# Performance work log

Hardware: AMD Instinct MI355X
Metric: run time of the kernel (lower is better)

## Reference

```python
import jax, jax.numpy as jnp
import numpy as np


def euler_xyz_to_matrix(angles):
    # pytorch3d euler_angles_to_matrix(angles, 'XYZ') = R_X(a0) @ R_Y(a1) @ R_Z(a2)
    ax, ay, az = angles[..., 0], angles[..., 1], angles[..., 2]
    cx, sx = jnp.cos(ax), jnp.sin(ax)
    cy, sy = jnp.cos(ay), jnp.sin(ay)
    cz, sz = jnp.cos(az), jnp.sin(az)
    one = jnp.ones_like(ax)
    zero = jnp.zeros_like(ax)
    Rx = jnp.stack([one, zero, zero, zero, cx, -sx, zero, sx, cx], axis=-1).reshape(*ax.shape, 3, 3)
    Ry = jnp.stack([cy, zero, sy, zero, one, zero, -sy, zero, cy], axis=-1).reshape(*ax.shape, 3, 3)
    Rz = jnp.stack([cz, -sz, zero, sz, cz, zero, zero, zero, one], axis=-1).reshape(*ax.shape, 3, 3)
    return Rx @ Ry @ Rz


def chamfer_bidir(x, y):
    # x, y: [R, I, N, 3]. Squared-distance chamfer, mean point reduction, per (R,I) batch.
    x2 = jnp.sum(x * x, axis=-1)  # [R,I,N]
    y2 = jnp.sum(y * y, axis=-1)  # [R,I,N]
    # d2[r,i,n,m] = |x_n - y_m|^2
    d2 = x2[..., :, None] + y2[..., None, :] - 2.0 * jnp.einsum('rind,rimd->rinm', x, y)
    cham_x = jnp.mean(jnp.min(d2, axis=-1), axis=-1)  # x -> nearest y
    cham_y = jnp.mean(jnp.min(d2, axis=-2), axis=-1)  # y -> nearest x
    return cham_x + cham_y  # [R, I]


def setup_inputs() -> dict:
    key = jax.random.key(0)
    k1, k2, k3, k4 = jax.random.split(key, 4)
    R, I, N = 4, 16, 2048
    source_points = jax.random.normal(k1, (R, I, N, 3), dtype=jnp.float32)
    target_points = jax.random.normal(k2, (I, N, 3), dtype=jnp.float32)
    rotation = 0.1 * jax.random.normal(k3, (R, I, 3), dtype=jnp.float32)
    translation = 0.1 * jax.random.normal(k4, (R, I, 3), dtype=jnp.float32)
    scale = jnp.ones((R, I), dtype=jnp.float32)
    return {
        'source_points': source_points,
        'target_points': target_points,
        'rotation': rotation,
        'translation': translation,
        'scale': scale,
    }


def reference(source_points, target_points, rotation, translation, scale):
    R, I, N, _ = source_points.shape
    rot = euler_xyz_to_matrix(rotation)  # [R,I,3,3]
    # Transform per original: 4x4 matrix with rows [:3,:] scaled by `scale`,
    # so p' = scale * (rot @ p + translation).
    transformed = scale[..., None, None] * (
        jnp.einsum('rind,rikd->rink', source_points, rot) + translation[..., None, :]
    )  # [R,I,N,3]
    # target_points [I,N,3] broadcast to [R,I,N,3] (original repeats along R)
    target = jnp.broadcast_to(target_points[None], transformed.shape)
    # original calls chamfer_distance(target, transformed): x=target, y=transformed
    return chamfer_bidir(target, transformed)  # [R, I]
```

## Files before the change

kernel.cpp:

```cpp
#include <hip/hip_runtime.h>
#include <math.h>

#define RDIM 4
#define IDIM 16
#define NPAIR 64
#define NPTS 2048
#define THREADS 256
#define ROWSB 256
#define RBLK (NPTS / ROWSB)
#define TILES (NPTS / 32)
#define SCRS 68
#define ONEBF 0x3F80u

typedef __attribute__((ext_vector_type(8))) short bf16x8;
typedef __attribute__((ext_vector_type(16))) float f32x16;
typedef __attribute__((ext_vector_type(4))) float f32x4;

__device__ __forceinline__ unsigned int f2bf(float f) {
    union { float f; unsigned int u; } v; v.f = f;
    return (v.u + 0x7FFFu + ((v.u >> 16) & 1u)) >> 16;
}
__device__ __forceinline__ float bf2f(unsigned int h) {
    union { unsigned int u; float f; } v; v.u = h << 16; return v.f;
}

__device__ __forceinline__ void make_rot(const float* __restrict__ rotv, int pair,
                                         float& r00, float& r01, float& r02,
                                         float& r10, float& r11, float& r12,
                                         float& r20, float& r21, float& r22) {
    const float ax = rotv[pair * 3 + 0];
    const float ay = rotv[pair * 3 + 1];
    const float az = rotv[pair * 3 + 2];
    float sx, cx, sy, cy, sz, cz;
    sincosf(ax, &sx, &cx);
    sincosf(ay, &sy, &cy);
    sincosf(az, &sz, &cz);
    r00 = cy * cz;                r01 = -cy * sz;               r02 = sy;
    r10 = cx * sz + sx * sy * cz; r11 = cx * cz - sx * sy * sz; r12 = -sx * cy;
    r20 = sx * sz - cx * sy * cz; r21 = sx * cz + cx * sy * sz; r22 = cx * cy;
}

__device__ __forceinline__ uint4 brec(float v0, float v1, float v2) {
    const float b0 = -2.0f * v0, b1 = -2.0f * v1, b2 = -2.0f * v2;
    const unsigned int h0 = f2bf(b0), h1 = f2bf(b1), h2 = f2bf(b2);
    const unsigned int l0 = f2bf(b0 - bf2f(h0));
    const unsigned int l1 = f2bf(b1 - bf2f(h1));
    const unsigned int l2 = f2bf(b2 - bf2f(h2));
    const float n2 = v0 * v0 + v1 * v1 + v2 * v2;
    const unsigned int nh = f2bf(n2), nl = f2bf(n2 - bf2f(nh));
    return make_uint4(h0 | (h1 << 16), h2 | (l0 << 16), l1 | (l2 << 16), nh | (nl << 16));
}
__device__ __forceinline__ void arec(float q0, float q1, float q2, uint4& a0, uint4& a1) {
    const unsigned int h0 = f2bf(q0), h1 = f2bf(q1), h2 = f2bf(q2);
    const unsigned int l0 = f2bf(q0 - bf2f(h0));
    const unsigned int l1 = f2bf(q1 - bf2f(h1));
    const unsigned int l2 = f2bf(q2 - bf2f(h2));
    a0 = make_uint4(h0 | (h1 << 16), h2 | (l0 << 16), l1 | (l2 << 16), ONEBF);
    a1 = make_uint4(l0 | (l1 << 16), l2 | (h0 << 16), h1 | (h2 << 16), ONEBF << 16);
}

__global__ __launch_bounds__(THREADS)
void prep(const float* __restrict__ src, const float* __restrict__ tgt,
          const float* __restrict__ rotv, const float* __restrict__ trav,
          const float* __restrict__ scal,
          uint4* __restrict__ Yb, uint4* __restrict__ Ya,
          uint4* __restrict__ Xb, uint4* __restrict__ Xa)
{
    const int b = blockIdx.x;
    const int tid = threadIdx.x;
    if (b < NPAIR) {
        const int pair = b;
        float r00, r01, r02, r10, r11, r12, r20, r21, r22;
        make_rot(rotv, pair, r00, r01, r02, r10, r11, r12, r20, r21, r22);
        const float t0 = trav[pair * 3 + 0];
        const float t1 = trav[pair * 3 + 1];
        const float t2 = trav[pair * 3 + 2];
        const float s  = scal[pair];
        const float* __restrict__ srcp = src + (size_t)pair * NPTS * 3;
#pragma unroll
        for (int u = 0; u < NPTS / THREADS; ++u) {
            const int m = u * THREADS + tid;
            const float p0 = srcp[m * 3 + 0];
            const float p1 = srcp[m * 3 + 1];
            const float p2 = srcp[m * 3 + 2];
            const float y0 = s * fmaf(r00, p0, fmaf(r01, p1, fmaf(r02, p2, t0)));
            const float y1 = s * fmaf(r10, p0, fmaf(r11, p1, fmaf(r12, p2, t1)));
            const float y2 = s * fmaf(r20, p0, fmaf(r21, p1, fmaf(r22, p2, t2)));
            Yb[(size_t)pair * NPTS + m] = brec(y0, y1, y2);
            uint4 a0, a1;
            arec(y0, y1, y2, a0, a1);
            Ya[((size_t)pair * NPTS + m) * 2 + 0] = a0;
            Ya[((size_t)pair * NPTS + m) * 2 + 1] = a1;
        }
    } else {
        const int i = b - NPAIR;
        const float* __restrict__ tgtp = tgt + (size_t)i * NPTS * 3;
#pragma unroll
        for (int u = 0; u < NPTS / THREADS; ++u) {
            const int m = u * THREADS + tid;
            const float x0 = tgtp[m * 3 + 0];
            const float x1 = tgtp[m * 3 + 1];
            const float x2 = tgtp[m * 3 + 2];
            Xb[(size_t)i * NPTS + m] = brec(x0, x1, x2);
            uint4 a0, a1;
            arec(x0, x1, x2, a0, a1);
            Xa[((size_t)i * NPTS + m) * 2 + 0] = a0;
            Xa[((size_t)i * NPTS + m) * 2 + 1] = a1;
        }
    }
}

__global__ __launch_bounds__(THREADS, 3)
void chamfer_main(const uint4* __restrict__ Yb, const uint4* __restrict__ Ya,
                  const uint4* __restrict__ Xb, const uint4* __restrict__ Xa,
                  float* __restrict__ out)
{
    __shared__ alignas(16) unsigned char smem[34816 + 8192];
    __shared__ float wsum[4];
    unsigned short* sB = (unsigned short*)smem;
    float* scratch = (float*)smem;
    unsigned short* sA = (unsigned short*)(smem + 34816);

    const int pair  = blockIdx.x;
    const int rb    = blockIdx.y;
    const int passB = blockIdx.z;
    const int i     = pair & (IDIM - 1);
    const int tid   = threadIdx.x;
    const int lane  = tid & 63;
    const int w     = tid >> 6;
    const int c31   = lane & 31;
    const int h     = lane >> 5;

    const uint4* __restrict__ gB = (passB == 0) ? (Yb + (size_t)pair * NPTS)
                                                : (Xb + (size_t)i * NPTS);
    const uint4* __restrict__ gA = (passB == 0)
        ? (Xa + ((size_t)i * NPTS + rb * ROWSB) * 2)
        : (Ya + ((size_t)pair * NPTS + rb * ROWSB) * 2);

#pragma unroll
    for (int j = 0; j < 8; ++j)
        ((uint4*)sB)[j * THREADS + tid] = gB[j * THREADS + tid];
    ((uint4*)sA)[tid] = gA[tid];
    ((uint4*)sA)[THREADS + tid] = gA[THREADS + tid];
    __syncthreads();

    bf16x8 af[2];
    af[0] = *(const bf16x8*)&sA[(w * 64 + c31) * 16 + h * 8];
    af[1] = *(const bf16x8*)&sA[(w * 64 + 32 + c31) * 16 + h * 8];

    float mn[2][16];
#pragma unroll
    for (int rt = 0; rt < 2; ++rt)
#pragma unroll
        for (int j = 0; j < 16; ++j) mn[rt][j] = 3.4e38f;

    const f32x16 zero16 = {0,0,0,0, 0,0,0,0, 0,0,0,0, 0,0,0,0};

#pragma unroll 4
    for (int t = 0; t < TILES; ++t) {
        const bf16x8 bf = *(const bf16x8*)&sB[(t * 32 + c31) * 8];
        const f32x16 d0 = __builtin_amdgcn_mfma_f32_32x32x16_bf16(af[0], bf, zero16, 0, 0, 0);
        const f32x16 d1 = __builtin_amdgcn_mfma_f32_32x32x16_bf16(af[1], bf, zero16, 0, 0, 0);
#pragma unroll
        for (int j = 0; j < 16; ++j) {
            mn[0][j] = fminf(mn[0][j], d0[j]);
            mn[1][j] = fminf(mn[1][j], d1[j]);
        }
    }
    __syncthreads();

#pragma unroll
    for (int rt = 0; rt < 2; ++rt)
#pragma unroll
        for (int g2 = 0; g2 < 4; ++g2) {
            const int rowb = rt * 32 + 8 * g2 + 4 * h;
            f32x4 v4;
            v4[0] = mn[rt][g2 * 4 + 0];
            v4[1] = mn[rt][g2 * 4 + 1];
            v4[2] = mn[rt][g2 * 4 + 2];
            v4[3] = mn[rt][g2 * 4 + 3];
            *(f32x4*)&scratch[(w * 32 + c31) * SCRS + rowb] = v4;
        }
    __syncthreads();

    float m = scratch[(w * 32) * SCRS + lane];
#pragma unroll
    for (int c = 1; c < 32; ++c)
        m = fminf(m, scratch[(w * 32 + c) * SCRS + lane]);

    const unsigned short* ar = &sA[tid * 16];
    const float q0 = bf2f(ar[0]) + bf2f(ar[3]);
    const float q1 = bf2f(ar[1]) + bf2f(ar[4]);
    const float q2 = bf2f(ar[2]) + bf2f(ar[5]);
    float v = m + q0 * q0 + q1 * q1 + q2 * q2;

#pragma unroll
    for (int off = 32; off > 0; off >>= 1)
        v += __shfl_down(v, off, 64);
    if (lane == 0) wsum[w] = v;
    __syncthreads();
    if (tid == 0) {
        const float tot = wsum[0] + wsum[1] + wsum[2] + wsum[3];
        atomicAdd(&out[pair], tot * (1.0f / NPTS));
    }
}

extern "C" void kernel_launch(void* const* d_in, const int* in_sizes, int n_in,
                              void* d_out, int out_size, void* d_ws, size_t ws_size,
                              hipStream_t stream) {
    const float* src  = (const float*)d_in[0];
    const float* tgt  = (const float*)d_in[1];
    const float* rotv = (const float*)d_in[2];
    const float* trav = (const float*)d_in[3];
    const float* scal = (const float*)d_in[4];
    float* out = (float*)d_out;

    char* ws = (char*)d_ws;
    uint4* Yb = (uint4*)ws;
    uint4* Ya = (uint4*)(ws + (size_t)NPAIR * NPTS * 16);
    uint4* Xb = (uint4*)(ws + (size_t)NPAIR * NPTS * 48);
    uint4* Xa = (uint4*)(ws + (size_t)NPAIR * NPTS * 48 + (size_t)IDIM * NPTS * 16);

    hipMemsetAsync(out, 0, NPAIR * sizeof(float), stream);

    prep<<<NPAIR + IDIM, THREADS, 0, stream>>>(src, tgt, rotv, trav, scal, Yb, Ya, Xb, Xa);

    dim3 grid(NPAIR, RBLK, 2);
    chamfer_main<<<grid, THREADS, 0, stream>>>(Yb, Ya, Xb, Xa, out);
}
```

Baseline: 86.91 us.

## Split prep across more blocks, raise occupancy, pair MFMA tiles with min3, swizzle scratch

The prep kernel is split into four segments per batch so more blocks participate in the transform and bf16 packing. The main kernel shrinks the scratch stride to 64 and uses an XOR swizzle to avoid LDS bank conflicts, which lets shared memory drop enough to target four blocks per CU. The inner loop processes two tiles per iteration and folds them with three-input min to cut VALU min ops. Requesting higher occupancy may push register pressure and risk spills.

```diff
diff --git a/kernel.cpp b/kernel.cpp
--- a/kernel.cpp
+++ b/kernel.cpp
@@ -9,12 +9,17 @@
 #define ROWSB 256
 #define RBLK (NPTS / ROWSB)
 #define TILES (NPTS / 32)
-#define SCRS 68
+#define SCRS 64
+#define PSPLIT 4
 #define ONEBF 0x3F80u
 
 typedef __attribute__((ext_vector_type(8))) short bf16x8;
 typedef __attribute__((ext_vector_type(16))) float f32x16;
 typedef __attribute__((ext_vector_type(4))) float f32x4;
+
+__device__ __forceinline__ float min3f(float a, float b, float c) {
+    return fminf(a, fminf(b, c));
+}
 
 __device__ __forceinline__ unsigned int f2bf(float f) {
     union { float f; unsigned int u; } v; v.f = f;
@@ -66,8 +71,10 @@
           uint4* __restrict__ Yb, uint4* __restrict__ Ya,
           uint4* __restrict__ Xb, uint4* __restrict__ Xa)
 {
-    const int b = blockIdx.x;
+    const int b   = blockIdx.x;
+    const int seg = blockIdx.y;
     const int tid = threadIdx.x;
+    const int m0  = seg * (NPTS / PSPLIT);
     if (b < NPAIR) {
         const int pair = b;
         float r00, r01, r02, r10, r11, r12, r20, r21, r22;
@@ -78,8 +85,8 @@
         const float s  = scal[pair];
         const float* __restrict__ srcp = src + (size_t)pair * NPTS * 3;
 #pragma unroll
-        for (int u = 0; u < NPTS / THREADS; ++u) {
-            const int m = u * THREADS + tid;
+        for (int u = 0; u < NPTS / THREADS / PSPLIT; ++u) {
+            const int m = m0 + u * THREADS + tid;
             const float p0 = srcp[m * 3 + 0];
             const float p1 = srcp[m * 3 + 1];
             const float p2 = srcp[m * 3 + 2];
@@ -96,8 +103,8 @@
         const int i = b - NPAIR;
         const float* __restrict__ tgtp = tgt + (size_t)i * NPTS * 3;
 #pragma unroll
-        for (int u = 0; u < NPTS / THREADS; ++u) {
-            const int m = u * THREADS + tid;
+        for (int u = 0; u < NPTS / THREADS / PSPLIT; ++u) {
+            const int m = m0 + u * THREADS + tid;
             const float x0 = tgtp[m * 3 + 0];
             const float x1 = tgtp[m * 3 + 1];
             const float x2 = tgtp[m * 3 + 2];
@@ -110,16 +117,16 @@
     }
 }
 
-__global__ __launch_bounds__(THREADS, 3)
+__global__ __launch_bounds__(THREADS, 4)
 void chamfer_main(const uint4* __restrict__ Yb, const uint4* __restrict__ Ya,
                   const uint4* __restrict__ Xb, const uint4* __restrict__ Xa,
                   float* __restrict__ out)
 {
-    __shared__ alignas(16) unsigned char smem[34816 + 8192];
+    __shared__ alignas(16) unsigned char smem[32768 + 8192];
     __shared__ float wsum[4];
     unsigned short* sB = (unsigned short*)smem;
     float* scratch = (float*)smem;
-    unsigned short* sA = (unsigned short*)(smem + 34816);
+    unsigned short* sA = (unsigned short*)(smem + 32768);
 
     const int pair  = blockIdx.x;
     const int rb    = blockIdx.y;
@@ -156,16 +163,20 @@
 
     const f32x16 zero16 = {0,0,0,0, 0,0,0,0, 0,0,0,0, 0,0,0,0};
 
-#pragma unroll 4
-    for (int t = 0; t < TILES; ++t) {
-        const bf16x8 bf = *(const bf16x8*)&sB[(t * 32 + c31) * 8];
-        const f32x16 d0 = __builtin_amdgcn_mfma_f32_32x32x16_bf16(af[0], bf, zero16, 0, 0, 0);
-        const f32x16 d1 = __builtin_amdgcn_mfma_f32_32x32x16_bf16(af[1], bf, zero16, 0, 0, 0);
-#pragma unroll
-        for (int j = 0; j < 16; ++j) {
-            mn[0][j] = fminf(mn[0][j], d0[j]);
-            mn[1][j] = fminf(mn[1][j], d1[j]);
-        }
+#pragma unroll 2
+    for (int t = 0; t < TILES; t += 2) {
+        const bf16x8 bfA = *(const bf16x8*)&sB[((t + 0) * 32 + c31) * 8];
+        const bf16x8 bfB = *(const bf16x8*)&sB[((t + 1) * 32 + c31) * 8];
+        const f32x16 a0 = __builtin_amdgcn_mfma_f32_32x32x16_bf16(af[0], bfA, zero16, 0, 0, 0);
+        const f32x16 b0 = __builtin_amdgcn_mfma_f32_32x32x16_bf16(af[0], bfB, zero16, 0, 0, 0);
+#pragma unroll
+        for (int j = 0; j < 16; ++j)
+            mn[0][j] = min3f(mn[0][j], a0[j], b0[j]);
+        const f32x16 a1 = __builtin_amdgcn_mfma_f32_32x32x16_bf16(af[1], bfA, zero16, 0, 0, 0);
+        const f32x16 b1 = __builtin_amdgcn_mfma_f32_32x32x16_bf16(af[1], bfB, zero16, 0, 0, 0);
+#pragma unroll
+        for (int j = 0; j < 16; ++j)
+            mn[1][j] = min3f(mn[1][j], a1[j], b1[j]);
     }
     __syncthreads();
 
@@ -173,7 +184,7 @@
     for (int rt = 0; rt < 2; ++rt)
 #pragma unroll
         for (int g2 = 0; g2 < 4; ++g2) {
-            const int rowb = rt * 32 + 8 * g2 + 4 * h;
+            const int rowb = (rt * 32 + 8 * g2 + 4 * h) ^ ((c31 & 7) << 2);
             f32x4 v4;
             v4[0] = mn[rt][g2 * 4 + 0];
             v4[1] = mn[rt][g2 * 4 + 1];
@@ -183,10 +194,12 @@
         }
     __syncthreads();
 
-    float m = scratch[(w * 32) * SCRS + lane];
-#pragma unroll
-    for (int c = 1; c < 32; ++c)
-        m = fminf(m, scratch[(w * 32 + c) * SCRS + lane]);
+    float m = fminf(scratch[(w * 32 + 0) * SCRS + lane],
+                    scratch[(w * 32 + 31) * SCRS + (lane ^ ((31 & 7) << 2))]);
+#pragma unroll
+    for (int c = 1; c < 31; c += 2)
+        m = min3f(m, scratch[(w * 32 + c) * SCRS + (lane ^ ((c & 7) << 2))],
+                     scratch[(w * 32 + c + 1) * SCRS + (lane ^ (((c + 1) & 7) << 2))]);
 
     const unsigned short* ar = &sA[tid * 16];
     const float q0 = bf2f(ar[0]) + bf2f(ar[3]);
@@ -223,7 +236,8 @@
 
     hipMemsetAsync(out, 0, NPAIR * sizeof(float), stream);
 
-    prep<<<NPAIR + IDIM, THREADS, 0, stream>>>(src, tgt, rotv, trav, scal, Yb, Ya, Xb, Xa);
+    dim3 pgrid(NPAIR + IDIM, PSPLIT);
+    prep<<<pgrid, THREADS, 0, stream>>>(src, tgt, rotv, trav, scal, Yb, Ya, Xb, Xa);
 
     dim3 grid(NPAIR, RBLK, 2);
     chamfer_main<<<grid, THREADS, 0, stream>>>(Yb, Ya, Xb, Xa, out);
```

Result: slower. 103.9 us (+19.6%).
